# Performance work log

Hardware: AMD Instinct MI355X
Metric: run time of the kernel (lower is better)

## Reference

```python
import jax, jax.numpy as jnp
import numpy as np

B, T, D = 2, 2048, 1024
H, Dh = 16, 64


def setup_inputs() -> dict:
    key = jax.random.key(0)
    ks = jax.random.split(key, 5)
    s = 0.02
    return {
        "x": jax.random.normal(ks[0], (B, T, D), dtype=jnp.float32),
        "attention_mask": jnp.ones((B, T), dtype=jnp.int32),
        "Wq": jax.random.normal(ks[1], (D, H * Dh), dtype=jnp.float32) * s,
        "Wk": jax.random.normal(ks[2], (D, H * Dh), dtype=jnp.float32) * s,
        "Wv": jax.random.normal(ks[3], (D, H * Dh), dtype=jnp.float32) * s,
        "Wo": jax.random.normal(ks[4], (H * Dh, D), dtype=jnp.float32) * s,
    }


def reference(x, attention_mask, Wq, Wk, Wv, Wo):
    scale = Dh ** -0.5
    # projections: [B,T,H,Dh]
    q = (x @ Wq).reshape(B, T, H, Dh)
    k = (x @ Wk).reshape(B, T, H, Dh)
    v = (x @ Wv).reshape(B, T, H, Dh)
    # scores: [B,H,T,T]
    attn = jnp.einsum("bqhd,bkhd->bhqk", q, k) * scale
    mask = attention_mask.astype(jnp.float32)[:, None, None, :]  # [B,1,1,T]
    attn = attn + (1.0 - mask) * -1e9
    attn = jax.nn.softmax(attn, axis=-1)
    # dropout p=0.0 (eval) -> identity
    out = jnp.einsum("bhqk,bkhd->bqhd", attn, v).reshape(B, T, H * Dh)
    return out @ Wo
```

## Files before the change

### kernel.cpp

```cpp
#include <hip/hip_runtime.h>
#include <stdint.h>

typedef unsigned short u16;
typedef unsigned int u32;

constexpr int CB = 2, CT = 2048, CH = 16, CDH = 64, CD = 1024;

typedef __attribute__((ext_vector_type(8))) short bf16x8;
typedef __attribute__((ext_vector_type(4))) float f32x4;

typedef __attribute__((address_space(1))) const u32 as1_cu32;
typedef __attribute__((address_space(3))) u32 as3_u32;

__device__ __forceinline__ void gload_lds16(const void* g, void* l) {
  __builtin_amdgcn_global_load_lds((as1_cu32*)g, (as3_u32*)l, 16, 0, 0);
}

__device__ __forceinline__ u16 f2b(float f) {
  u32 x = __float_as_uint(f);
  u32 r = (x + 0x7fffu + ((x >> 16) & 1u)) >> 16;
  return (u16)r;
}

#if __has_builtin(__builtin_amdgcn_cvt_pk_bf16_f32)
typedef __attribute__((ext_vector_type(2))) __bf16 v2bf;
__device__ __forceinline__ u32 pk2(float a, float b) {
  v2bf r = __builtin_amdgcn_cvt_pk_bf16_f32(a, b);
  union { v2bf v; u32 u; } cv; cv.v = r; return cv.u;
}
#else
__device__ __forceinline__ u32 pk2(float a, float b) {
  return (u32)f2b(a) | ((u32)f2b(b) << 16);
}
#endif

__device__ __forceinline__ void store_out(u16* p, float v) { *p = f2b(v); }
__device__ __forceinline__ void store_out(float* p, float v) { *p = v; }

__global__ __launch_bounds__(256) void cast_bf16_k(const float* __restrict__ x,
                                                   u16* __restrict__ o, int n4) {
  int i = blockIdx.x * 256 + threadIdx.x;
  if (i < n4) {
    float4 v = ((const float4*)x)[i];
    ushort4 r;
    r.x = f2b(v.x); r.y = f2b(v.y); r.z = f2b(v.z); r.w = f2b(v.w);
    ((ushort4*)o)[i] = r;
  }
}

__global__ __launch_bounds__(256) void transpose_cast_k(const float* __restrict__ W,
                                                        u16* __restrict__ Wt) {
  __shared__ float tile[32][33];
  int bx = blockIdx.x * 32, by = blockIdx.y * 32;
  int tx = threadIdx.x & 31, ty = threadIdx.x >> 5;
  #pragma unroll
  for (int i = ty; i < 32; i += 8) tile[i][tx] = W[(size_t)(by + i) * CD + bx + tx];
  __syncthreads();
  #pragma unroll
  for (int i = ty; i < 32; i += 8)
    Wt[(size_t)(bx + i) * CD + by + tx] = f2b(tile[tx][i]);
}

template <typename OT>
__global__ __launch_bounds__(256) void gemm_bt_k(const u16* __restrict__ A,
                                                 const u16* __restrict__ Bt,
                                                 OT* __restrict__ Cout,
                                                 int K, size_t subStride) {
  __shared__ __align__(16) u16 As[128 * 32];
  __shared__ __align__(16) u16 Bs[128 * 32];
  int t = threadIdx.x;
  int lane = t & 63, w = t >> 6;
  int m = lane & 15, quad = lane >> 4;
  int wrow = w >> 1, wcol = w & 1;
  int m0 = blockIdx.y * 128, n0 = blockIdx.x * 128;

  f32x4 acc[4][4];
  #pragma unroll
  for (int i = 0; i < 4; i++)
    #pragma unroll
    for (int j = 0; j < 4; j++) acc[i][j] = (f32x4){0.f, 0.f, 0.f, 0.f};

  for (int k0 = 0; k0 < K; k0 += 32) {
    __syncthreads();
    #pragma unroll
    for (int p = 0; p < 2; p++) {
      int idx = p * 256 + t;
      int row = idx >> 2, c = idx & 3;
      int cc = c ^ (row & 3);
      gload_lds16(A + (size_t)(m0 + row) * K + k0 + cc * 8,
                  As + (size_t)(p * 256 + (t & 192)) * 8);
      gload_lds16(Bt + (size_t)(n0 + row) * K + k0 + cc * 8,
                  Bs + (size_t)(p * 256 + (t & 192)) * 8);
    }
    __syncthreads();
    bf16x8 af[4], bfr[4];
    #pragma unroll
    for (int mt = 0; mt < 4; mt++) {
      int r = wrow * 64 + mt * 16 + m;
      af[mt] = *(const bf16x8*)&As[r * 32 + ((quad ^ (r & 3)) * 8)];
    }
    #pragma unroll
    for (int nt = 0; nt < 4; nt++) {
      int r = wcol * 64 + nt * 16 + m;
      bfr[nt] = *(const bf16x8*)&Bs[r * 32 + ((quad ^ (r & 3)) * 8)];
    }
    #pragma unroll
    for (int mt = 0; mt < 4; mt++)
      #pragma unroll
      for (int nt = 0; nt < 4; nt++)
        acc[mt][nt] = __builtin_amdgcn_mfma_f32_16x16x32_bf16(af[mt], bfr[nt],
                                                              acc[mt][nt], 0, 0, 0);
  }

  #pragma unroll
  for (int mt = 0; mt < 4; mt++) {
    #pragma unroll
    for (int nt = 0; nt < 4; nt++) {
      int c = n0 + wcol * 64 + nt * 16 + m;
      OT* outp = Cout + (size_t)(c >> 10) * subStride + (c & 1023);
      #pragma unroll
      for (int rr = 0; rr < 4; rr++) {
        int r = m0 + wrow * 64 + mt * 16 + quad * 4 + rr;
        store_out(outp + (size_t)r * CD, acc[mt][nt][rr]);
      }
    }
  }
}

__global__ __launch_bounds__(128) void attn_k(const u16* __restrict__ Qb,
                                              const u16* __restrict__ Kb,
                                              const u16* __restrict__ Vb,
                                              const int* __restrict__ mask,
                                              u16* __restrict__ Ob) {
  __shared__ __align__(16) u16 Qs[64 * 64];
  __shared__ __align__(16) u16 Ks[64 * 64];
  __shared__ __align__(16) u32 VsD[64 * 36];
  __shared__ __align__(16) u16 Ps[64 * 72];
  __shared__ u16 biasS[2048];
  __shared__ float Lf[64];

  int t = threadIdx.x, lane = t & 63, w = t >> 6;
  int m = lane & 15, quad = lane >> 4;
  int qt = blockIdx.x, h = blockIdx.y, b = blockIdx.z;
  const float scale = 0.125f;

  const u16* Qg = Qb + ((size_t)(b * CT + qt * 64)) * CD + h * CDH;
  #pragma unroll
  for (int p = 0; p < 4; p++) {
    int idx = p * 128 + t;
    int row = idx >> 3, c = idx & 7;
    int cc = c ^ (row & 7);
    gload_lds16(Qg + (size_t)row * CD + cc * 8, Qs + (size_t)(p * 128 + (t & 64)) * 8);
  }

  const int* mk = mask + b * CT;
  int localAny = 0;
  for (int i = t; i < CT; i += 128) {
    int mv = mk[i];
    biasS[i] = mv ? (u16)0 : f2b(-1.0e9f);
    localAny |= (mv == 0);
  }
  int anyM = __syncthreads_or(localAny);
  __syncthreads();

  bf16x8 qbf[2][2];
  #pragma unroll
  for (int nt = 0; nt < 2; nt++) {
    int qrow = w * 32 + nt * 16 + m;
    #pragma unroll
    for (int kf = 0; kf < 2; kf++) {
      int ch = (4 * kf + quad) ^ (qrow & 7);
      qbf[nt][kf] = *(const bf16x8*)&Qs[qrow * 64 + ch * 8];
    }
  }

  f32x4 oacc[2][4];
  float lp[2] = {0.f, 0.f};
  #pragma unroll
  for (int nt = 0; nt < 2; nt++)
    #pragma unroll
    for (int j = 0; j < 4; j++) oacc[nt][j] = (f32x4){0.f, 0.f, 0.f, 0.f};

  for (int kv = 0; kv < CT; kv += 64) {
    __syncthreads();
    const u16* Kg = Kb + ((size_t)(b * CT + kv)) * CD + h * CDH;
    #pragma unroll
    for (int p = 0; p < 4; p++) {
      int idx = p * 128 + t;
      int row = idx >> 3, c = idx & 7;
      int cc = c ^ (row & 7);
      gload_lds16(Kg + (size_t)row * CD + cc * 8, Ks + (size_t)(p * 128 + (t & 64)) * 8);
    }
    #pragma unroll
    for (int rep = 0; rep < 2; rep++) {
      int u = rep * 128 + t;
      int pr = u >> 3, dg = u & 7;
      const u16* Vg = Vb + ((size_t)(b * CT + kv + 2 * pr)) * CD + h * CDH + dg * 8;
      uint4 va = *(const uint4*)Vg;
      uint4 vb2 = *(const uint4*)(Vg + CD);
      const u32* pa = (const u32*)&va;
      const u32* pb = (const u32*)&vb2;
      u32* dst = VsD + 288 * dg + (pr ^ (dg << 2));
      #pragma unroll
      for (int j = 0; j < 8; j++) {
        u32 lo_dw = pa[j >> 1], hi_dw = pb[j >> 1];
        u32 pk = (j & 1) ? __builtin_amdgcn_perm(hi_dw, lo_dw, 0x07060302u)
                         : __builtin_amdgcn_perm(hi_dw, lo_dw, 0x05040100u);
        dst[j * 36] = pk;
      }
    }
    __syncthreads();

    f32x4 s[2][4];
    #pragma unroll
    for (int jt = 0; jt < 4; jt++) {
      s[0][jt] = (f32x4){0.f, 0.f, 0.f, 0.f};
      s[1][jt] = (f32x4){0.f, 0.f, 0.f, 0.f};
      int key = jt * 16 + m;
      #pragma unroll
      for (int kf = 0; kf < 2; kf++) {
        int ch = (4 * kf + quad) ^ (key & 7);
        bf16x8 af = *(const bf16x8*)&Ks[key * 64 + ch * 8];
        s[0][jt] = __builtin_amdgcn_mfma_f32_16x16x32_bf16(af, qbf[0][kf], s[0][jt], 0, 0, 0);
        s[1][jt] = __builtin_amdgcn_mfma_f32_16x16x32_bf16(af, qbf[1][kf], s[1][jt], 0, 0, 0);
      }
    }

    #pragma unroll
    for (int nt = 0; nt < 2; nt++) {
      int qrow = w * 32 + nt * 16 + m;
      #pragma unroll
      for (int jt = 0; jt < 4; jt++) {
        float b0 = 0.f, b1 = 0.f, b2 = 0.f, b3 = 0.f;
        if (anyM) {
          uint2 bw = *(const uint2*)&biasS[kv + jt * 16 + quad * 4];
          b0 = __uint_as_float(bw.x << 16);
          b1 = __uint_as_float(bw.x & 0xffff0000u);
          b2 = __uint_as_float(bw.y << 16);
          b3 = __uint_as_float(bw.y & 0xffff0000u);
        }
        float p0 = __expf(fminf(fmaf(s[nt][jt][0], scale, b0), 30.f));
        float p1 = __expf(fminf(fmaf(s[nt][jt][1], scale, b1), 30.f));
        float p2 = __expf(fminf(fmaf(s[nt][jt][2], scale, b2), 30.f));
        float p3 = __expf(fminf(fmaf(s[nt][jt][3], scale, b3), 30.f));
        lp[nt] += (p0 + p1) + (p2 + p3);
        uint2 pw;
        pw.x = pk2(p0, p1);
        pw.y = pk2(p2, p3);
        *(uint2*)&Ps[qrow * 72 + jt * 16 + quad * 4] = pw;
      }
    }

    bf16x8 pf[2][2];
    #pragma unroll
    for (int nt = 0; nt < 2; nt++)
      #pragma unroll
      for (int kf2 = 0; kf2 < 2; kf2++)
        pf[nt][kf2] = *(const bf16x8*)&Ps[(w * 32 + nt * 16 + m) * 72 + kf2 * 32 + quad * 8];
    #pragma unroll
    for (int jt2 = 0; jt2 < 4; jt2++) {
      int row = jt2 * 16 + m;
      int X = ((row >> 3) & 7) << 2;
      #pragma unroll
      for (int kf2 = 0; kf2 < 2; kf2++) {
        const u32* vp = VsD + row * 36 + ((16 * kf2 + 4 * quad) ^ X);
        bf16x8 vf = *(const bf16x8*)vp;
        oacc[0][jt2] = __builtin_amdgcn_mfma_f32_16x16x32_bf16(pf[0][kf2], vf, oacc[0][jt2], 0, 0, 0);
        oacc[1][jt2] = __builtin_amdgcn_mfma_f32_16x16x32_bf16(pf[1][kf2], vf, oacc[1][jt2], 0, 0, 0);
      }
    }
  }

  #pragma unroll
  for (int nt = 0; nt < 2; nt++) {
    float l = lp[nt];
    l += __shfl_xor(l, 16, 64);
    l += __shfl_xor(l, 32, 64);
    if (lane < 16) Lf[w * 32 + nt * 16 + lane] = l;
  }
  __syncthreads();
  #pragma unroll
  for (int nt = 0; nt < 2; nt++) {
    #pragma unroll
    for (int r = 0; r < 4; r++) {
      float linv = 1.f / Lf[w * 32 + nt * 16 + quad * 4 + r];
      int tg = qt * 64 + w * 32 + nt * 16 + quad * 4 + r;
      size_t base = ((size_t)(b * CT + tg)) * CD + h * CDH;
      #pragma unroll
      for (int jt2 = 0; jt2 < 4; jt2++)
        Ob[base + jt2 * 16 + m] = f2b(oacc[nt][jt2][r] * linv);
    }
  }
}

extern "C" void kernel_launch(void* const* d_in, const int* in_sizes, int n_in,
                              void* d_out, int out_size, void* d_ws, size_t ws_size,
                              hipStream_t stream) {
  const float* x  = (const float*)d_in[0];
  const int* mask = (const int*)d_in[1];
  const float* Wq = (const float*)d_in[2];
  const float* Wk = (const float*)d_in[3];
  const float* Wv = (const float*)d_in[4];
  const float* Wo = (const float*)d_in[5];
  float* out = (float*)d_out;

  u16* Xb   = (u16*)d_ws;
  u16* Wqkv = Xb + (size_t)4096 * 1024;
  u16* WoT  = Wqkv + (size_t)3072 * 1024;
  u16* Qb   = WoT + (size_t)1024 * 1024;
  u16* Ob   = Qb + (size_t)3 * 4096 * 1024;

  cast_bf16_k<<<4096, 256, 0, stream>>>(x, Xb, 1048576);
  transpose_cast_k<<<dim3(32, 32), 256, 0, stream>>>(Wq, Wqkv);
  transpose_cast_k<<<dim3(32, 32), 256, 0, stream>>>(Wk, Wqkv + (size_t)1024 * 1024);
  transpose_cast_k<<<dim3(32, 32), 256, 0, stream>>>(Wv, Wqkv + (size_t)2 * 1024 * 1024);
  transpose_cast_k<<<dim3(32, 32), 256, 0, stream>>>(Wo, WoT);
  gemm_bt_k<u16><<<dim3(24, 32), 256, 0, stream>>>(Xb, Wqkv, Qb, 1024,
                                                   (size_t)4096 * 1024);
  attn_k<<<dim3(32, 16, 2), 128, 0, stream>>>(Qb, Qb + (size_t)4096 * 1024,
                                              Qb + (size_t)2 * 4096 * 1024, mask, Ob);
  gemm_bt_k<float><<<dim3(8, 32), 256, 0, stream>>>(Ob, WoT, out, 1024, 0);
}
```

Baseline: 235.6 us.

## Split attention over KV halves with 32x32 MFMA, register-resident P, and combine pass

Merges the x cast and the four weight transpose-casts into a single prep launch. Rewrites attention to use 256-thread blocks covering 128 queries, with 32x32x16 MFMAs and Q held in registers. P now stays in registers, reshuffled by cross-lane swaps instead of going through LDS, and the next V tile is prefetched into registers. The KV range is split into two halves across blocks, and a new combine kernel merges the partial outputs weighted by their row sums. This doubles grid parallelism and cuts LDS traffic, at the cost of extra partial-output memory traffic, bf16 rounding of the partials, and one more launch.

```diff
diff --git a/kernel.cpp b/kernel.cpp
--- a/kernel.cpp
+++ b/kernel.cpp
@@ -8,6 +8,7 @@
 
 typedef __attribute__((ext_vector_type(8))) short bf16x8;
 typedef __attribute__((ext_vector_type(4))) float f32x4;
+typedef __attribute__((ext_vector_type(16))) float f32x16;
 
 typedef __attribute__((address_space(1))) const u32 as1_cu32;
 typedef __attribute__((address_space(3))) u32 as3_u32;
@@ -34,31 +35,48 @@
 }
 #endif
 
+__device__ __forceinline__ float b2f(u32 lo16) { return __uint_as_float(lo16 << 16); }
+
 __device__ __forceinline__ void store_out(u16* p, float v) { *p = f2b(v); }
 __device__ __forceinline__ void store_out(float* p, float v) { *p = v; }
 
-__global__ __launch_bounds__(256) void cast_bf16_k(const float* __restrict__ x,
-                                                   u16* __restrict__ o, int n4) {
-  int i = blockIdx.x * 256 + threadIdx.x;
-  if (i < n4) {
+__device__ __forceinline__ void plswap(u32& a, u32& b, int hf) {
+  u32 ta = (u32)__shfl_xor((int)a, 32, 64);
+  u32 tb = (u32)__shfl_xor((int)b, 32, 64);
+  u32 na = hf ? tb : a;
+  u32 nb = hf ? b : ta;
+  a = na; b = nb;
+}
+
+__global__ __launch_bounds__(256) void prep_k(const float* __restrict__ x,
+                                              const float* __restrict__ Wq,
+                                              const float* __restrict__ Wk,
+                                              const float* __restrict__ Wv,
+                                              const float* __restrict__ Wo,
+                                              u16* __restrict__ Xb,
+                                              u16* __restrict__ Wt) {
+  __shared__ float tile[32][33];
+  int bid = blockIdx.x, t = threadIdx.x;
+  if (bid < 4096) {
+    int i = bid * 256 + t;
     float4 v = ((const float4*)x)[i];
     ushort4 r;
     r.x = f2b(v.x); r.y = f2b(v.y); r.z = f2b(v.z); r.w = f2b(v.w);
-    ((ushort4*)o)[i] = r;
-  }
-}
-
-__global__ __launch_bounds__(256) void transpose_cast_k(const float* __restrict__ W,
-                                                        u16* __restrict__ Wt) {
-  __shared__ float tile[32][33];
-  int bx = blockIdx.x * 32, by = blockIdx.y * 32;
-  int tx = threadIdx.x & 31, ty = threadIdx.x >> 5;
-  #pragma unroll
-  for (int i = ty; i < 32; i += 8) tile[i][tx] = W[(size_t)(by + i) * CD + bx + tx];
-  __syncthreads();
-  #pragma unroll
-  for (int i = ty; i < 32; i += 8)
-    Wt[(size_t)(bx + i) * CD + by + tx] = f2b(tile[tx][i]);
+    ((ushort4*)Xb)[i] = r;
+  } else {
+    int tid2 = bid - 4096;
+    int mat = tid2 >> 10, b2 = tid2 & 1023;
+    const float* W = (mat == 0) ? Wq : (mat == 1) ? Wk : (mat == 2) ? Wv : Wo;
+    u16* dst = Wt + (size_t)mat * 1048576;
+    int bx = (b2 & 31) * 32, by = (b2 >> 5) * 32;
+    int tx = t & 31, ty = t >> 5;
+    #pragma unroll
+    for (int i = ty; i < 32; i += 8) tile[i][tx] = W[(size_t)(by + i) * CD + bx + tx];
+    __syncthreads();
+    #pragma unroll
+    for (int i = ty; i < 32; i += 8)
+      dst[(size_t)(bx + i) * CD + by + tx] = f2b(tile[tx][i]);
+  }
 }
 
 template <typename OT>
@@ -127,80 +145,61 @@
   }
 }
 
-__global__ __launch_bounds__(128) void attn_k(const u16* __restrict__ Qb,
-                                              const u16* __restrict__ Kb,
-                                              const u16* __restrict__ Vb,
-                                              const int* __restrict__ mask,
-                                              u16* __restrict__ Ob) {
-  __shared__ __align__(16) u16 Qs[64 * 64];
+__global__ __launch_bounds__(256, 4) void attn_k(const u16* __restrict__ Qb,
+                                                 const u16* __restrict__ Kb,
+                                                 const u16* __restrict__ Vb,
+                                                 const int* __restrict__ mask,
+                                                 u16* __restrict__ Opart,
+                                                 float* __restrict__ Lpart) {
   __shared__ __align__(16) u16 Ks[64 * 64];
   __shared__ __align__(16) u32 VsD[64 * 36];
-  __shared__ __align__(16) u16 Ps[64 * 72];
-  __shared__ u16 biasS[2048];
-  __shared__ float Lf[64];
 
   int t = threadIdx.x, lane = t & 63, w = t >> 6;
-  int m = lane & 15, quad = lane >> 4;
-  int qt = blockIdx.x, h = blockIdx.y, b = blockIdx.z;
-  const float scale = 0.125f;
-
-  const u16* Qg = Qb + ((size_t)(b * CT + qt * 64)) * CD + h * CDH;
-  #pragma unroll
-  for (int p = 0; p < 4; p++) {
-    int idx = p * 128 + t;
-    int row = idx >> 3, c = idx & 7;
-    int cc = c ^ (row & 7);
-    gload_lds16(Qg + (size_t)row * CD + cc * 8, Qs + (size_t)(p * 128 + (t & 64)) * 8);
-  }
-
-  const int* mk = mask + b * CT;
+  int c32 = lane & 31, hf = lane >> 5;
+  int qt = blockIdx.x, head = blockIdx.y;
+  int b = blockIdx.z & 1, half = blockIdx.z >> 1;
+  int kv0 = half * 1024;
+  int gid = (b * 16 + head) * 16 + qt;
+
+  const u16* Qg = Qb + ((size_t)(b * CT + qt * 128 + w * 32 + c32)) * CD + head * CDH;
+  bf16x8 qbf[4];
+  #pragma unroll
+  for (int kc = 0; kc < 4; kc++)
+    qbf[kc] = *(const bf16x8*)(Qg + kc * 16 + hf * 8);
+
+  const int* mk = mask + b * CT + kv0;
   int localAny = 0;
-  for (int i = t; i < CT; i += 128) {
-    int mv = mk[i];
-    biasS[i] = mv ? (u16)0 : f2b(-1.0e9f);
-    localAny |= (mv == 0);
-  }
+  for (int i = t; i < 1024; i += 256) localAny |= (mk[i] == 0);
   int anyM = __syncthreads_or(localAny);
-  __syncthreads();
-
-  bf16x8 qbf[2][2];
-  #pragma unroll
-  for (int nt = 0; nt < 2; nt++) {
-    int qrow = w * 32 + nt * 16 + m;
-    #pragma unroll
-    for (int kf = 0; kf < 2; kf++) {
-      int ch = (4 * kf + quad) ^ (qrow & 7);
-      qbf[nt][kf] = *(const bf16x8*)&Qs[qrow * 64 + ch * 8];
-    }
-  }
-
-  f32x4 oacc[2][4];
-  float lp[2] = {0.f, 0.f};
-  #pragma unroll
-  for (int nt = 0; nt < 2; nt++)
-    #pragma unroll
-    for (int j = 0; j < 4; j++) oacc[nt][j] = (f32x4){0.f, 0.f, 0.f, 0.f};
-
-  for (int kv = 0; kv < CT; kv += 64) {
-    __syncthreads();
-    const u16* Kg = Kb + ((size_t)(b * CT + kv)) * CD + h * CDH;
-    #pragma unroll
-    for (int p = 0; p < 4; p++) {
-      int idx = p * 128 + t;
-      int row = idx >> 3, c = idx & 7;
-      int cc = c ^ (row & 7);
-      gload_lds16(Kg + (size_t)row * CD + cc * 8, Ks + (size_t)(p * 128 + (t & 64)) * 8);
-    }
-    #pragma unroll
-    for (int rep = 0; rep < 2; rep++) {
-      int u = rep * 128 + t;
-      int pr = u >> 3, dg = u & 7;
-      const u16* Vg = Vb + ((size_t)(b * CT + kv + 2 * pr)) * CD + h * CDH + dg * 8;
-      uint4 va = *(const uint4*)Vg;
-      uint4 vb2 = *(const uint4*)(Vg + CD);
+
+  f32x16 oacc[2];
+  #pragma unroll
+  for (int dt = 0; dt < 2; dt++)
+    #pragma unroll
+    for (int r = 0; r < 16; r++) oacc[dt][r] = 0.f;
+  float lp = 0.f;
+
+  const u16* Kg0 = Kb + ((size_t)(b * CT + kv0)) * CD + head * CDH;
+  const u16* Vg0 = Vb + ((size_t)(b * CT + kv0)) * CD + head * CDH;
+
+  int vpr = t >> 3, vdg = t & 7;
+  const u16* VgT = Vg0 + (size_t)(2 * vpr) * CD + vdg * 8;
+  uint4 va = *(const uint4*)VgT;
+  uint4 vb2 = *(const uint4*)(VgT + CD);
+
+  for (int kv = 0; kv < 1024; kv += 64) {
+    __syncthreads();
+    #pragma unroll
+    for (int p = 0; p < 2; p++) {
+      int idx = p * 256 + t;
+      int row = idx >> 3, cc = (idx & 7) ^ (row & 7);
+      gload_lds16(Kg0 + (size_t)(kv + row) * CD + cc * 8,
+                  Ks + (size_t)(p * 256 + (t & 192)) * 8);
+    }
+    {
       const u32* pa = (const u32*)&va;
       const u32* pb = (const u32*)&vb2;
-      u32* dst = VsD + 288 * dg + (pr ^ (dg << 2));
+      u32* dst = VsD + (size_t)vdg * 288 + (vpr ^ (vdg << 2));
       #pragma unroll
       for (int j = 0; j < 8; j++) {
         u32 lo_dw = pa[j >> 1], hi_dw = pb[j >> 1];
@@ -210,87 +209,100 @@
       }
     }
     __syncthreads();
-
-    f32x4 s[2][4];
-    #pragma unroll
-    for (int jt = 0; jt < 4; jt++) {
-      s[0][jt] = (f32x4){0.f, 0.f, 0.f, 0.f};
-      s[1][jt] = (f32x4){0.f, 0.f, 0.f, 0.f};
-      int key = jt * 16 + m;
-      #pragma unroll
-      for (int kf = 0; kf < 2; kf++) {
-        int ch = (4 * kf + quad) ^ (key & 7);
-        bf16x8 af = *(const bf16x8*)&Ks[key * 64 + ch * 8];
-        s[0][jt] = __builtin_amdgcn_mfma_f32_16x16x32_bf16(af, qbf[0][kf], s[0][jt], 0, 0, 0);
-        s[1][jt] = __builtin_amdgcn_mfma_f32_16x16x32_bf16(af, qbf[1][kf], s[1][jt], 0, 0, 0);
-      }
-    }
-
-    #pragma unroll
-    for (int nt = 0; nt < 2; nt++) {
-      int qrow = w * 32 + nt * 16 + m;
-      #pragma unroll
-      for (int jt = 0; jt < 4; jt++) {
-        float b0 = 0.f, b1 = 0.f, b2 = 0.f, b3 = 0.f;
+    if (kv + 64 < 1024) {
+      VgT = Vg0 + (size_t)(kv + 64 + 2 * vpr) * CD + vdg * 8;
+      va = *(const uint4*)VgT;
+      vb2 = *(const uint4*)(VgT + CD);
+    }
+
+    #pragma unroll
+    for (int kt = 0; kt < 2; kt++) {
+      f32x16 sv;
+      #pragma unroll
+      for (int r = 0; r < 16; r++) sv[r] = 0.f;
+      int key = kt * 32 + c32;
+      #pragma unroll
+      for (int kc = 0; kc < 4; kc++) {
+        int ch = kc * 2 + hf;
+        bf16x8 af = *(const bf16x8*)&Ks[key * 64 + ((ch ^ (key & 7)) * 8)];
+        sv = __builtin_amdgcn_mfma_f32_32x32x16_bf16(af, qbf[kc], sv, 0, 0, 0);
+      }
+      float pv[16];
+      #pragma unroll
+      for (int r = 0; r < 16; r++) {
+        float xs = sv[r] * 0.125f;
         if (anyM) {
-          uint2 bw = *(const uint2*)&biasS[kv + jt * 16 + quad * 4];
-          b0 = __uint_as_float(bw.x << 16);
-          b1 = __uint_as_float(bw.x & 0xffff0000u);
-          b2 = __uint_as_float(bw.y << 16);
-          b3 = __uint_as_float(bw.y & 0xffff0000u);
+          int mi = kv + kt * 32 + (r & 3) + 8 * (r >> 2) + 4 * hf;
+          xs += mk[mi] ? 0.f : -1.0e9f;
         }
-        float p0 = __expf(fminf(fmaf(s[nt][jt][0], scale, b0), 30.f));
-        float p1 = __expf(fminf(fmaf(s[nt][jt][1], scale, b1), 30.f));
-        float p2 = __expf(fminf(fmaf(s[nt][jt][2], scale, b2), 30.f));
-        float p3 = __expf(fminf(fmaf(s[nt][jt][3], scale, b3), 30.f));
-        lp[nt] += (p0 + p1) + (p2 + p3);
-        uint2 pw;
-        pw.x = pk2(p0, p1);
-        pw.y = pk2(p2, p3);
-        *(uint2*)&Ps[qrow * 72 + jt * 16 + quad * 4] = pw;
-      }
-    }
-
-    bf16x8 pf[2][2];
-    #pragma unroll
-    for (int nt = 0; nt < 2; nt++)
-      #pragma unroll
-      for (int kf2 = 0; kf2 < 2; kf2++)
-        pf[nt][kf2] = *(const bf16x8*)&Ps[(w * 32 + nt * 16 + m) * 72 + kf2 * 32 + quad * 8];
-    #pragma unroll
-    for (int jt2 = 0; jt2 < 4; jt2++) {
-      int row = jt2 * 16 + m;
-      int X = ((row >> 3) & 7) << 2;
-      #pragma unroll
-      for (int kf2 = 0; kf2 < 2; kf2++) {
-        const u32* vp = VsD + row * 36 + ((16 * kf2 + 4 * quad) ^ X);
-        bf16x8 vf = *(const bf16x8*)vp;
-        oacc[0][jt2] = __builtin_amdgcn_mfma_f32_16x16x32_bf16(pf[0][kf2], vf, oacc[0][jt2], 0, 0, 0);
-        oacc[1][jt2] = __builtin_amdgcn_mfma_f32_16x16x32_bf16(pf[1][kf2], vf, oacc[1][jt2], 0, 0, 0);
-      }
-    }
-  }
-
-  #pragma unroll
-  for (int nt = 0; nt < 2; nt++) {
-    float l = lp[nt];
-    l += __shfl_xor(l, 16, 64);
-    l += __shfl_xor(l, 32, 64);
-    if (lane < 16) Lf[w * 32 + nt * 16 + lane] = l;
-  }
-  __syncthreads();
-  #pragma unroll
-  for (int nt = 0; nt < 2; nt++) {
-    #pragma unroll
-    for (int r = 0; r < 4; r++) {
-      float linv = 1.f / Lf[w * 32 + nt * 16 + quad * 4 + r];
-      int tg = qt * 64 + w * 32 + nt * 16 + quad * 4 + r;
-      size_t base = ((size_t)(b * CT + tg)) * CD + h * CDH;
-      #pragma unroll
-      for (int jt2 = 0; jt2 < 4; jt2++)
-        Ob[base + jt2 * 16 + m] = f2b(oacc[nt][jt2][r] * linv);
-    }
-  }
+        pv[r] = __expf(fminf(xs, 30.f));
+        lp += pv[r];
+      }
+      u32 pk[8];
+      #pragma unroll
+      for (int i = 0; i < 8; i++) pk[i] = pk2(pv[2 * i], pv[2 * i + 1]);
+      #pragma unroll
+      for (int c = 0; c < 2; c++) {
+        u32 d0 = pk[4 * c + 0], d2 = pk[4 * c + 2];
+        u32 d1 = pk[4 * c + 1], d3 = pk[4 * c + 3];
+        plswap(d0, d2, hf);
+        plswap(d1, d3, hf);
+        union { u32 u[4]; bf16x8 v; } pf;
+        pf.u[0] = d0; pf.u[1] = d1; pf.u[2] = d2; pf.u[3] = d3;
+        int prb = kt * 16 + c * 8 + hf * 4;
+        #pragma unroll
+        for (int dt = 0; dt < 2; dt++) {
+          int d = dt * 32 + c32;
+          const u32* vp = VsD + d * 36 + (prb ^ ((d >> 3) << 2));
+          bf16x8 vf = *(const bf16x8*)vp;
+          oacc[dt] = __builtin_amdgcn_mfma_f32_32x32x16_bf16(vf, pf.v, oacc[dt], 0, 0, 0);
+        }
+      }
+    }
+  }
+
+  float lT = lp + __shfl_xor(lp, 32, 64);
+  float linv = 1.f / lT;
+  u16* Op = Opart + ((size_t)(half * 512 + gid) * 128 + w * 32 + c32) * 64;
+  #pragma unroll
+  for (int dt = 0; dt < 2; dt++) {
+    #pragma unroll
+    for (int g = 0; g < 4; g++) {
+      float o0 = oacc[dt][4 * g + 0] * linv, o1 = oacc[dt][4 * g + 1] * linv;
+      float o2 = oacc[dt][4 * g + 2] * linv, o3 = oacc[dt][4 * g + 3] * linv;
+      uint2 pw;
+      pw.x = pk2(o0, o1);
+      pw.y = pk2(o2, o3);
+      *(uint2*)(Op + dt * 32 + 8 * g + 4 * hf) = pw;
+    }
+  }
+  if (lane < 32) Lpart[(size_t)(half * 512 + gid) * 128 + w * 32 + lane] = lT;
+}
+
+__global__ __launch_bounds__(256) void combine_k(const u16* __restrict__ Opart,
+                                                 const float* __restrict__ Lpart,
+                                                 u16* __restrict__ Ob) {
+  int fid = blockIdx.x * 256 + threadIdx.x;
+  int gid = fid >> 11;
+  int rem = fid & 2047;
+  int r = rem >> 4, d = (rem & 15) * 4;
+  int b = gid >> 8, head = (gid >> 4) & 15, qt = gid & 15;
+  size_t i0 = ((size_t)gid * 128 + r) * 64 + d;
+  size_t i1 = ((size_t)(512 + gid) * 128 + r) * 64 + d;
+  uint2 A = *(const uint2*)(Opart + i0);
+  uint2 Bv = *(const uint2*)(Opart + i1);
+  float la = Lpart[gid * 128 + r], lb = Lpart[(512 + gid) * 128 + r];
+  float inv = 1.f / (la + lb);
+  float wa = la * inv, wb = lb * inv;
+  float o0 = wa * b2f(A.x & 0xffffu) + wb * b2f(Bv.x & 0xffffu);
+  float o1 = wa * b2f(A.x >> 16) + wb * b2f(Bv.x >> 16);
+  float o2 = wa * b2f(A.y & 0xffffu) + wb * b2f(Bv.y & 0xffffu);
+  float o3 = wa * b2f(A.y >> 16) + wb * b2f(Bv.y >> 16);
+  uint2 pw;
+  pw.x = pk2(o0, o1);
+  pw.y = pk2(o2, o3);
+  size_t trow = (size_t)b * CT + qt * 128 + r;
+  *(uint2*)(Ob + trow * CD + head * CDH + d) = pw;
 }
 
 extern "C" void kernel_launch(void* const* d_in, const int* in_sizes, int n_in,
@@ -304,20 +316,20 @@
   const float* Wo = (const float*)d_in[5];
   float* out = (float*)d_out;
 
-  u16* Xb   = (u16*)d_ws;
-  u16* Wqkv = Xb + (size_t)4096 * 1024;
-  u16* WoT  = Wqkv + (size_t)3072 * 1024;
-  u16* Qb   = WoT + (size_t)1024 * 1024;
-  u16* Ob   = Qb + (size_t)3 * 4096 * 1024;
-
-  cast_bf16_k<<<4096, 256, 0, stream>>>(x, Xb, 1048576);
-  transpose_cast_k<<<dim3(32, 32), 256, 0, stream>>>(Wq, Wqkv);
-  transpose_cast_k<<<dim3(32, 32), 256, 0, stream>>>(Wk, Wqkv + (size_t)1024 * 1024);
-  transpose_cast_k<<<dim3(32, 32), 256, 0, stream>>>(Wv, Wqkv + (size_t)2 * 1024 * 1024);
-  transpose_cast_k<<<dim3(32, 32), 256, 0, stream>>>(Wo, WoT);
+  u16* Xb    = (u16*)d_ws;
+  u16* Wqkv  = Xb + (size_t)4096 * 1024;
+  u16* WoT   = Wqkv + (size_t)3072 * 1024;
+  u16* Qb    = Wqkv + (size_t)4096 * 1024;
+  u16* Ob    = Qb + (size_t)3 * 4096 * 1024;
+  u16* Opart = Ob + (size_t)4096 * 1024;
+  float* Lpart = (float*)(Opart + (size_t)2 * 512 * 128 * 64);
+
+  prep_k<<<8192, 256, 0, stream>>>(x, Wq, Wk, Wv, Wo, Xb, Wqkv);
   gemm_bt_k<u16><<<dim3(24, 32), 256, 0, stream>>>(Xb, Wqkv, Qb, 1024,
                                                    (size_t)4096 * 1024);
-  attn_k<<<dim3(32, 16, 2), 128, 0, stream>>>(Qb, Qb + (size_t)4096 * 1024,
-                                              Qb + (size_t)2 * 4096 * 1024, mask, Ob);
+  attn_k<<<dim3(16, 16, 4), 256, 0, stream>>>(Qb, Qb + (size_t)4096 * 1024,
+                                              Qb + (size_t)2 * 4096 * 1024, mask,
+                                              Opart, Lpart);
+  combine_k<<<4096, 256, 0, stream>>>(Opart, Lpart, Ob);
   gemm_bt_k<float><<<dim3(8, 32), 256, 0, stream>>>(Ob, WoT, out, 1024, 0);
 }
```

Result: faster. 220.3 us (-6.5%).
